# Kernel optimization log

Measured on AMD Instinct MI355X. Metric: run time of the kernel, lower is better.

## Reference

```python
import jax, jax.numpy as jnp
import numpy as np

N, E = 25000, 400000
D_NODE, D_EDGE_IN, D_EH, D_H, D_DUAL = 128, 16, 128, 256, 128


def layer_norm(x, g, b, eps=1e-5):
    mu = jnp.mean(x, axis=-1, keepdims=True)
    var = jnp.mean((x - mu) ** 2, axis=-1, keepdims=True)
    return (x - mu) * jax.lax.rsqrt(var + eps) * g + b


def setup_inputs() -> dict:
    key = jax.random.key(0)
    ks = jax.random.split(key, 20)

    def w(k, shape):
        return (jax.random.normal(k, shape, dtype=jnp.float32) * 0.05)

    inp = {
        "node_embedding": jax.random.normal(ks[0], (N, D_NODE), dtype=jnp.float32),
        "edge_index": jax.random.randint(ks[1], (2, E), 0, N, dtype=jnp.int64),
        "edge_attr": jax.random.normal(ks[2], (E, D_EDGE_IN), dtype=jnp.float32),
        "dual_node_emb": jax.random.normal(ks[3], (E, D_DUAL), dtype=jnp.float32),
        "atom_reactivity_logits": jax.random.normal(ks[4], (N,), dtype=jnp.float32),
        "W_be1": w(ks[5], (D_EDGE_IN, D_EH)), "b_be1": jnp.zeros((D_EH,), jnp.float32),
        "g_be1": jnp.ones((D_EH,), jnp.float32), "bb_be1": jnp.zeros((D_EH,), jnp.float32),
        "W_be2": w(ks[6], (D_EH, D_EH)), "b_be2": jnp.zeros((D_EH,), jnp.float32),
        "g_be2": jnp.ones((D_EH,), jnp.float32), "bb_be2": jnp.zeros((D_EH,), jnp.float32),
        "W_be3": w(ks[7], (D_EH, D_EH)), "b_be3": jnp.zeros((D_EH,), jnp.float32),
        "g_be3": jnp.ones((D_EH,), jnp.float32), "bb_be3": jnp.zeros((D_EH,), jnp.float32),
        # DualGraphBondReactivityPredictor
        "W_d1": w(ks[8], (D_DUAL, D_H)), "b_d1": jnp.zeros((D_H,), jnp.float32),
        "W_d2": w(ks[9], (D_H, D_H)), "b_d2": jnp.zeros((D_H,), jnp.float32),
        "W_do": w(ks[10], (D_H, 1)), "b_do": jnp.zeros((1,), jnp.float32),
        # main head: in = 2*D_NODE + D_EH + 3 = 387
        "W_f1": w(ks[11], (2 * D_NODE + D_EH + 3, D_H)), "b_f1": jnp.zeros((D_H,), jnp.float32),
        "W_f2": w(ks[12], (D_H, D_H)), "b_f2": jnp.zeros((D_H,), jnp.float32),
        "W_bo": w(ks[13], (D_H, 1)), "b_bo": jnp.zeros((1,), jnp.float32),
    }
    return inp


def reference(node_embedding, edge_index, edge_attr, dual_node_emb, atom_reactivity_logits,
              W_be1, b_be1, g_be1, bb_be1, W_be2, b_be2, g_be2, bb_be2,
              W_be3, b_be3, g_be3, bb_be3,
              W_d1, b_d1, W_d2, b_d2, W_do, b_do,
              W_f1, b_f1, W_f2, b_f2, W_bo, b_bo):
    src, dst = edge_index[0], edge_index[1]

    # BondEmbedding (dropout = identity in eval mode)
    e = jax.nn.silu(layer_norm(edge_attr @ W_be1 + b_be1, g_be1, bb_be1))
    e = jax.nn.silu(layer_norm(e @ W_be2 + b_be2, g_be2, bb_be2))
    e = jax.nn.silu(layer_norm(e @ W_be3 + b_be3, g_be3, bb_be3))  # [E, D_EH]

    atom_p = jax.nn.sigmoid(atom_reactivity_logits)  # [N]
    p_src = atom_p[src][:, None]  # [E,1]
    p_dst = atom_p[dst][:, None]

    # dual-graph bond reactivity
    d = jax.nn.silu(dual_node_emb @ W_d1 + b_d1)
    d = jax.nn.silu(d @ W_d2 + b_d2)
    dual_p = jax.nn.sigmoid((d @ W_do + b_do)[:, 0])[:, None]  # [E,1]

    feats = jnp.concatenate(
        [node_embedding[src], node_embedding[dst], e, dual_p, p_src, p_dst], axis=-1
    )  # [E, 2*D_NODE + D_EH + 3]

    x = jax.nn.silu(feats @ W_f1 + b_f1)
    x = jax.nn.silu(x @ W_f2 + b_f2)
    return (x @ W_bo + b_bo)[:, 0]  # [E]
```

## Files before the change

### kernel.cpp

```cpp
#include <hip/hip_runtime.h>
#include <hip/hip_bf16.h>
#include <stdint.h>

typedef __attribute__((ext_vector_type(8))) short bf16x8;
typedef __attribute__((ext_vector_type(4))) float f32x4;
typedef __attribute__((ext_vector_type(4))) float float4v;

__device__ __forceinline__ uint16_t bfc(float x){
    __hip_bfloat16 h = __float2bfloat16(x);
    return __builtin_bit_cast(uint16_t, h);
}
__device__ __forceinline__ uint32_t pk2(float a, float b){
    return (uint32_t)bfc(a) | ((uint32_t)bfc(b) << 16);
}
__device__ __forceinline__ float fsigmoid(float x){ return 1.0f / (1.0f + __expf(-x)); }
__device__ __forceinline__ float fsilu(float x){ return x * fsigmoid(x); }

__device__ __forceinline__ bf16x8 pack8(float4v lo, float4v hi){
    bf16x8 r;
    r[0]=(short)bfc(lo[0]); r[1]=(short)bfc(lo[1]);
    r[2]=(short)bfc(lo[2]); r[3]=(short)bfc(lo[3]);
    r[4]=(short)bfc(hi[0]); r[5]=(short)bfc(hi[1]);
    r[6]=(short)bfc(hi[2]); r[7]=(short)bfc(hi[3]);
    return r;
}

#define SZ_BE1 4096
#define SZ_128 16384
#define SZ_D1  32768
#define SZ_D2  65536
#define SZ_F1  98304
#define OFF_BE1 0
#define OFF_BE2 (OFF_BE1 + SZ_BE1)
#define OFF_BE3 (OFF_BE2 + SZ_128)
#define OFF_D1  (OFF_BE3 + SZ_128)
#define OFF_D2  (OFF_D1 + SZ_D1)
#define OFF_F1  (OFF_D2 + SZ_D2)
#define OFF_F2  (OFF_F1 + SZ_F1)
#define WS_ELEMS (OFF_F2 + SZ_D2)

__device__ __forceinline__ int fragpos(int k, int c, int OUT){
    int kt = k >> 5, ct = c >> 4;
    int fid = kt * (OUT >> 4) + ct;
    int ln = ((k & 31) >> 3) * 16 + (c & 15);
    return fid * 512 + ln * 8 + (k & 7);
}

__global__ void __launch_bounds__(256)
prep_w(const float* __restrict__ Wbe1, const float* __restrict__ Wbe2,
       const float* __restrict__ Wbe3, const float* __restrict__ Wd1,
       const float* __restrict__ Wd2,  const float* __restrict__ Wf1,
       const float* __restrict__ Wf2,  uint16_t* __restrict__ ws){
    int t = blockIdx.x * 256 + threadIdx.x;
    if (t >= WS_ELEMS) return;
    if (t < OFF_BE2) {
        int u = t;            int k = u >> 7, c = u & 127;
        float v = (k < 16) ? Wbe1[k * 128 + c] : 0.0f;
        ws[OFF_BE1 + fragpos(k, c, 128)] = bfc(v);
    } else if (t < OFF_BE3) {
        int u = t - OFF_BE2;  int k = u >> 7, c = u & 127;
        ws[OFF_BE2 + fragpos(k, c, 128)] = bfc(Wbe2[u]);
    } else if (t < OFF_D1) {
        int u = t - OFF_BE3;  int k = u >> 7, c = u & 127;
        ws[OFF_BE3 + fragpos(k, c, 128)] = bfc(Wbe3[u]);
    } else if (t < OFF_D2) {
        int u = t - OFF_D1;   int k = u >> 8, c = u & 255;
        ws[OFF_D1 + fragpos(k, c, 256)] = bfc(Wd1[u]);
    } else if (t < OFF_F1) {
        int u = t - OFF_D2;   int k = u >> 8, c = u & 255;
        ws[OFF_D2 + fragpos(k, c, 256)] = bfc(Wd2[u]);
    } else if (t < OFF_F2) {
        int u = t - OFF_F1;   int k = u >> 8, c = u & 255;
        ws[OFF_F1 + fragpos(k, c, 256)] = bfc(Wf1[u]);
    } else {
        int u = t - OFF_F2;   int k = u >> 8, c = u & 255;
        ws[OFF_F2 + fragpos(k, c, 256)] = bfc(Wf2[u]);
    }
}

__global__ void __launch_bounds__(256)
prep_n(const float* __restrict__ src, uint16_t* __restrict__ dst, int n){
    int t = blockIdx.x * 256 + threadIdx.x;
    if (t < n) dst[t] = bfc(src[t]);
}

typedef const __attribute__((address_space(1))) void gas_void;
typedef __attribute__((address_space(3))) void las_void;
__device__ __forceinline__ void g2l16(const void* g, void* l){
    __builtin_amdgcn_global_load_lds((gas_void*)g, (las_void*)l, 16, 0, 0);
}

#define LDS_TOTAL 135168

__global__ void __launch_bounds__(1024) __attribute__((amdgpu_waves_per_eu(4, 4)))
bond_fast_kernel(const int* __restrict__ edge_index,
                 const float* __restrict__ edge_attr, const float* __restrict__ dual_emb,
                 const float* __restrict__ logits,
                 const float* __restrict__ b_be1, const float* __restrict__ g_be1, const float* __restrict__ bb_be1,
                 const float* __restrict__ b_be2, const float* __restrict__ g_be2, const float* __restrict__ bb_be2,
                 const float* __restrict__ b_be3, const float* __restrict__ g_be3, const float* __restrict__ bb_be3,
                 const float* __restrict__ b_d1, const float* __restrict__ b_d2,
                 const float* __restrict__ W_do, const float* __restrict__ b_do,
                 const float* __restrict__ W_f1, const float* __restrict__ b_f1,
                 const float* __restrict__ b_f2,
                 const float* __restrict__ W_bo, const float* __restrict__ b_bo,
                 const uint16_t* __restrict__ ws, float* __restrict__ out, int E)
{
    __shared__ char lds[LDS_TOTAL];
    const int t    = threadIdx.x;
    const int wave = t >> 6;
    const int lane = t & 63;
    const int li   = lane & 15, lg = lane >> 4;
    const int eg   = wave >> 1;
    const int ch   = wave & 1;
    const int e0b  = blockIdx.x * 128;

    char* bufE = lds;
    char* h256 = lds + 32768;
    uint16_t* wb0 = (uint16_t*)(lds + 98304);
    uint16_t* wb1 = (uint16_t*)(lds + 114688);
    float* ps  = (float*)(lds + 131072);
    float* pd  = (float*)(lds + 131584);
    int* sidx  = (int*)(lds + 132096);
    int* didx  = (int*)(lds + 132608);
    float* dpp = (float*)(lds + 133120);
    float* bop = (float*)(lds + 134144);

    const uint8_t*  wsb = (const uint8_t*)ws;
    const uint16_t* nbf = ws + WS_ELEMS;

    if (t < 128) {
        int e = e0b + t; if (e >= E) e = E - 1;
        int s_ = edge_index[e];
        int d_ = edge_index[E + e];
        sidx[t] = s_; didx[t] = d_;
        ps[t] = fsigmoid(logits[s_]);
        pd[t] = fsigmoid(logits[d_]);
    }

    int cur = 0;
    auto stageW16 = [&](int elemoff){
        uint8_t* dst = (uint8_t*)(cur ? wb0 : wb1) + t * 16;
        g2l16(wsb + (size_t)elemoff * 2 + t * 16, dst);
    };
    auto stageW8 = [&](int elemoff){
        if (t >= 512){
            int u = t - 512;
            uint8_t* dst = (uint8_t*)(cur ? wb0 : wb1) + u * 16;
            g2l16(wsb + (size_t)elemoff * 2 + u * 16, dst);
        }
    };
    auto stepend = [&](){ __syncthreads(); cur ^= 1; };
    auto curbuf  = [&]() -> const uint16_t* { return cur ? wb1 : wb0; };

    f32x4 acc[8];

    auto ldf = [&](const uint16_t* w, int fid) -> bf16x8 {
        return *(const bf16x8*)(w + fid * 512 + lane * 8);
    };
    auto grpBE = [&](const uint16_t* w, bf16x8 a0){
        #pragma unroll
        for (int ct = 0; ct < 8; ++ct){
            bf16x8 b = ldf(w, ct);
            acc[ct] = __builtin_amdgcn_mfma_f32_16x16x32_bf16(a0, b, acc[ct], 0, 0, 0);
        }
    };
    auto grp256 = [&](const uint16_t* w, bf16x8 a0){
        #pragma unroll
        for (int ct = 0; ct < 8; ++ct){
            bf16x8 b = ldf(w, ch * 8 + ct);
            acc[ct] = __builtin_amdgcn_mfma_f32_16x16x32_bf16(a0, b, acc[ct], 0, 0, 0);
        }
    };
    auto initBE = [&](const float* b){
        #pragma unroll
        for (int ct = 0; ct < 8; ++ct){
            float bv = b[li + 16 * ct];
            f32x4 iv = {bv, bv, bv, bv};
            acc[ct] = iv;
        }
    };
    auto init256 = [&](const float* b){
        #pragma unroll
        for (int ct = 0; ct < 8; ++ct){
            float bv = b[ch * 128 + ct * 16 + li];
            f32x4 iv = {bv, bv, bv, bv};
            acc[ct] = iv;
        }
    };
    auto eb_read = [&](int row, int kt) -> bf16x8 {
        int off = row * 256 + (kt * 32 + lg * 8) * 2;
        return *(const bf16x8*)(bufE + (off ^ ((row & 7) << 4)));
    };
    auto h2_read = [&](int row, int kt) -> bf16x8 {
        int off = row * 512 + (kt * 32 + lg * 8) * 2;
        return *(const bf16x8*)(h256 + (off ^ ((row & 7) << 4)));
    };
    auto lnstoreBE = [&](const float* g, const float* bb){
        #pragma unroll
        for (int r = 0; r < 4; ++r){
            float s = 0.f, q = 0.f;
            #pragma unroll
            for (int ct = 0; ct < 8; ++ct){ float v = acc[ct][r]; s += v; q += v*v; }
            s += __shfl_xor(s, 1); q += __shfl_xor(q, 1);
            s += __shfl_xor(s, 2); q += __shfl_xor(q, 2);
            s += __shfl_xor(s, 4); q += __shfl_xor(q, 4);
            s += __shfl_xor(s, 8); q += __shfl_xor(q, 8);
            float mu = s * 0.0078125f;
            float var = q * 0.0078125f - mu * mu;
            float rs = rsqrtf(var + 1e-5f);
            int row = wave * 16 + lg * 4 + r;
            int rswz = (row & 7) << 4;
            #pragma unroll
            for (int ct = 0; ct < 8; ++ct){
                int col = li + 16 * ct;
                float v = (acc[ct][r] - mu) * rs * g[col] + bb[col];
                int off = row * 256 + col * 2;
                *(uint16_t*)(bufE + (off ^ rswz)) = bfc(fsilu(v));
            }
        }
    };
    auto silustore256 = [&](){
        #pragma unroll
        for (int r = 0; r < 4; ++r){
            int row = eg * 16 + lg * 4 + r;
            int rswz = (row & 7) << 4;
            #pragma unroll
            for (int ct = 0; ct < 8; ++ct){
                int off = row * 512 + (ch * 128 + ct * 16 + li) * 2;
                *(uint16_t*)(h256 + (off ^ rswz)) = bfc(fsilu(acc[ct][r]));
            }
        }
    };

    if (t >= 512){
        int u = t - 512;
        g2l16(wsb + u * 16, (uint8_t*)wb0 + u * 16);
    }
    __syncthreads();

    {
        stageW8(OFF_BE2);
        if (wave < 8){
            bf16x8 aE = {0,0,0,0,0,0,0,0};
            if (lg < 2){
                int ea = e0b + wave * 16 + li; if (ea >= E) ea = E - 1;
                const float* pa = edge_attr + (size_t)ea * 16 + lg * 8;
                aE = pack8(*(const float4v*)pa, *(const float4v*)(pa + 4));
            }
            initBE(b_be1);
            grpBE(curbuf(), aE);
            lnstoreBE(g_be1, bb_be1);
        }
        stepend();
    }

    if (wave < 8) initBE(b_be2);
    #pragma unroll 1
    for (int kt = 0; kt < 4; ++kt){
        if (kt < 3) stageW8(OFF_BE2 + (kt + 1) * 4096);
        else        stageW8(OFF_BE3);
        if (wave < 8){
            grpBE(curbuf(), eb_read(wave * 16 + li, kt));
            if (kt == 3) lnstoreBE(g_be2, bb_be2);
        }
        stepend();
    }
    if (wave < 8) initBE(b_be3);
    #pragma unroll 1
    for (int kt = 0; kt < 4; ++kt){
        if (kt < 3) stageW8(OFF_BE3 + (kt + 1) * 4096);
        else        stageW16(OFF_D1);
        if (wave < 8){
            grpBE(curbuf(), eb_read(wave * 16 + li, kt));
            if (kt == 3) lnstoreBE(g_be3, bb_be3);
        }
        stepend();
    }

    init256(b_d1);
    #pragma unroll 1
    for (int kt = 0; kt < 4; ++kt){
        float4v va0, va1;
        {
            int ea = e0b + eg * 16 + li; if (ea >= E) ea = E - 1;
            const float* pa = dual_emb + (size_t)ea * 128 + kt * 32 + lg * 8;
            va0 = *(const float4v*)pa; va1 = *(const float4v*)(pa + 4);
        }
        if (kt < 3) stageW16(OFF_D1 + (kt + 1) * 8192);
        else        stageW16(OFF_D2);
        grp256(curbuf(), pack8(va0, va1));
        if (kt == 3) silustore256();
        stepend();
    }

    init256(b_d2);
    #pragma unroll 1
    for (int kt = 0; kt < 8; ++kt){
        if (kt < 7) stageW16(OFF_D2 + (kt + 1) * 8192);
        else        stageW16(OFF_F1);
        grp256(curbuf(), h2_read(eg * 16 + li, kt));
        if (kt == 7){
            #pragma unroll
            for (int r = 0; r < 4; ++r){
                float s = 0.f;
                #pragma unroll
                for (int ct = 0; ct < 8; ++ct)
                    s += fsilu(acc[ct][r]) * W_do[ch * 128 + ct * 16 + li];
                s += __shfl_xor(s, 1); s += __shfl_xor(s, 2);
                s += __shfl_xor(s, 4); s += __shfl_xor(s, 8);
                if (li == 0) dpp[ch * 128 + eg * 16 + lg * 4 + r] = s;
            }
        }
        stepend();
    }

    {
        {
            float bdo0 = b_do[0];
            float dvv[4], psr[4], pdr[4];
            #pragma unroll
            for (int r = 0; r < 4; ++r){
                int row = eg * 16 + lg * 4 + r;
                dvv[r] = fsigmoid(dpp[row] + dpp[128 + row] + bdo0);
                psr[r] = ps[row]; pdr[r] = pd[row];
            }
            #pragma unroll
            for (int ct = 0; ct < 8; ++ct){
                int col = ch * 128 + ct * 16 + li;
                float bv = b_f1[col];
                float t0 = W_f1[384 * 256 + col];
                float t1 = W_f1[385 * 256 + col];
                float t2 = W_f1[386 * 256 + col];
                #pragma unroll
                for (int r = 0; r < 4; ++r)
                    acc[ct][r] = bv + dvv[r]*t0 + psr[r]*t1 + pdr[r]*t2;
            }
        }
        int s0 = sidx[eg * 16 + li];
        int d0 = didx[eg * 16 + li];
        #pragma unroll 1
        for (int kt = 0; kt < 12; ++kt){
            bf16x8 a0;
            if (kt < 8){
                int ra = (kt < 4) ? s0 : d0;
                int ko = (kt & 3) * 32 + lg * 8;
                a0 = *(const bf16x8*)(nbf + (size_t)ra * 128 + ko);
            } else {
                a0 = eb_read(eg * 16 + li, kt - 8);
            }
            if (kt < 11) stageW16(OFF_F1 + (kt + 1) * 8192);
            else         stageW16(OFF_F2);
            grp256(curbuf(), a0);
            if (kt == 11) silustore256();
            stepend();
        }
    }

    init256(b_f2);
    #pragma unroll 1
    for (int kt = 0; kt < 8; ++kt){
        if (kt < 7) stageW16(OFF_F2 + (kt + 1) * 8192);
        grp256(curbuf(), h2_read(eg * 16 + li, kt));
        if (kt == 7){
            #pragma unroll
            for (int r = 0; r < 4; ++r){
                float s = 0.f;
                #pragma unroll
                for (int ct = 0; ct < 8; ++ct)
                    s += fsilu(acc[ct][r]) * W_bo[ch * 128 + ct * 16 + li];
                s += __shfl_xor(s, 1); s += __shfl_xor(s, 2);
                s += __shfl_xor(s, 4); s += __shfl_xor(s, 8);
                if (li == 0) bop[ch * 128 + eg * 16 + lg * 4 + r] = s;
            }
        } else {
            stepend();
        }
    }
    __syncthreads();
    if (t < 128){
        int e = e0b + t;
        if (e < E) out[e] = bop[t] + bop[128 + t] + b_bo[0];
    }
}

#define LDS_TOTAL_FB 135168
__global__ void __launch_bounds__(512) __attribute__((amdgpu_waves_per_eu(2, 2)))
bond_fused_kernel(const float* __restrict__ node_emb, const int* __restrict__ edge_index,
                  const float* __restrict__ edge_attr, const float* __restrict__ dual_emb,
                  const float* __restrict__ logits,
                  const float* __restrict__ W_be1, const float* __restrict__ b_be1,
                  const float* __restrict__ g_be1, const float* __restrict__ bb_be1,
                  const float* __restrict__ W_be2, const float* __restrict__ b_be2,
                  const float* __restrict__ g_be2, const float* __restrict__ bb_be2,
                  const float* __restrict__ W_be3, const float* __restrict__ b_be3,
                  const float* __restrict__ g_be3, const float* __restrict__ bb_be3,
                  const float* __restrict__ W_d1, const float* __restrict__ b_d1,
                  const float* __restrict__ W_d2, const float* __restrict__ b_d2,
                  const float* __restrict__ W_do, const float* __restrict__ b_do,
                  const float* __restrict__ W_f1, const float* __restrict__ b_f1,
                  const float* __restrict__ W_f2, const float* __restrict__ b_f2,
                  const float* __restrict__ W_bo, const float* __restrict__ b_bo,
                  float* __restrict__ out, int E)
{
    __shared__ char lds[LDS_TOTAL_FB];
    const int t    = threadIdx.x;
    const int wave = t >> 6;
    const int lane = t & 63;
    const int li   = lane & 15, lg = lane >> 4;
    const int eg   = wave >> 1;
    const int ch   = wave & 1;
    const int e0b  = blockIdx.x * 128;

    char* bufE = lds;
    char* h256 = lds + 32768;
    uint16_t* wb0 = (uint16_t*)(lds + 98304);
    uint16_t* wb1 = (uint16_t*)(lds + 114688);
    float* ps  = (float*)(lds + 131072);
    float* pd  = (float*)(lds + 131584);
    int* sidx  = (int*)(lds + 132096);
    int* didx  = (int*)(lds + 132608);
    float* dpp = (float*)(lds + 133120);
    float* bop = (float*)(lds + 134144);

    if (t < 128) {
        int e = e0b + t; if (e >= E) e = E - 1;
        int s_ = edge_index[e];
        int d_ = edge_index[E + e];
        sidx[t] = s_; didx[t] = d_;
        ps[t] = fsigmoid(logits[s_]);
        pd[t] = fsigmoid(logits[d_]);
    }

    float sr[2][8];
    auto issueW256 = [&](const float* W, int kbase){
        #pragma unroll
        for (int h = 0; h < 2; ++h){
            const float* p = W + (size_t)(kbase + lg * 8) * 256 + (wave + 8*h) * 16 + li;
            #pragma unroll
            for (int j = 0; j < 8; ++j) sr[h][j] = p[j * 256];
        }
    };
    auto issueW128 = [&](const float* W, int kbase, int K){
        const float* p = W + (size_t)(kbase + lg * 8) * 128 + wave * 16 + li;
        #pragma unroll
        for (int j = 0; j < 8; ++j)
            sr[0][j] = (kbase + lg * 8 + j < K) ? p[j * 128] : 0.f;
    };
    auto commitW = [&](uint16_t* dst, int nh){
        #pragma unroll
        for (int h = 0; h < 2; ++h){
            if (h < nh){
                uint4 w;
                w.x = pk2(sr[h][0], sr[h][1]); w.y = pk2(sr[h][2], sr[h][3]);
                w.z = pk2(sr[h][4], sr[h][5]); w.w = pk2(sr[h][6], sr[h][7]);
                *(uint4*)(dst + (wave + 8*h) * 512 + lane * 8) = w;
            }
        }
    };

    int cur = 0;
    auto stepend = [&](int mode){
        if (mode) commitW(cur ? wb0 : wb1, mode == 128 ? 1 : 2);
        __syncthreads();
        cur ^= 1;
    };
    auto curbuf = [&]() -> const uint16_t* { return cur ? wb1 : wb0; };

    f32x4 acc[2][8];

    auto ldf = [&](const uint16_t* w, int fid) -> bf16x8 {
        return *(const bf16x8*)(w + fid * 512 + lane * 8);
    };
    auto grpBE = [&](const uint16_t* w, bf16x8 a0){
        #pragma unroll
        for (int ct = 0; ct < 8; ++ct){
            bf16x8 b = ldf(w, ct);
            acc[0][ct] = __builtin_amdgcn_mfma_f32_16x16x32_bf16(a0, b, acc[0][ct], 0, 0, 0);
        }
    };
    auto grp256 = [&](const uint16_t* w, bf16x8 a0, bf16x8 a1){
        #pragma unroll
        for (int ct = 0; ct < 8; ++ct){
            bf16x8 b = ldf(w, ch * 8 + ct);
            acc[0][ct] = __builtin_amdgcn_mfma_f32_16x16x32_bf16(a0, b, acc[0][ct], 0, 0, 0);
            acc[1][ct] = __builtin_amdgcn_mfma_f32_16x16x32_bf16(a1, b, acc[1][ct], 0, 0, 0);
        }
    };
    auto initBE = [&](const float* b){
        #pragma unroll
        for (int ct = 0; ct < 8; ++ct){
            float bv = b[li + 16 * ct];
            f32x4 iv = {bv, bv, bv, bv};
            acc[0][ct] = iv;
        }
    };
    auto init256 = [&](const float* b){
        #pragma unroll
        for (int ct = 0; ct < 8; ++ct){
            float bv = b[ch * 128 + ct * 16 + li];
            f32x4 iv = {bv, bv, bv, bv};
            acc[0][ct] = iv; acc[1][ct] = iv;
        }
    };
    auto eb_read = [&](int row, int kt) -> bf16x8 {
        int off = row * 256 + (kt * 32 + lg * 8) * 2;
        return *(const bf16x8*)(bufE + (off ^ ((row & 7) << 4)));
    };
    auto h2_read = [&](int row, int kt) -> bf16x8 {
        int off = row * 512 + (kt * 32 + lg * 8) * 2;
        return *(const bf16x8*)(h256 + (off ^ ((row & 7) << 4)));
    };
    auto lnstoreBE = [&](const float* g, const float* bb){
        #pragma unroll
        for (int r = 0; r < 4; ++r){
            float s = 0.f, q = 0.f;
            #pragma unroll
            for (int ct = 0; ct < 8; ++ct){ float v = acc[0][ct][r]; s += v; q += v*v; }
            s += __shfl_xor(s, 1); q += __shfl_xor(q, 1);
            s += __shfl_xor(s, 2); q += __shfl_xor(q, 2);
            s += __shfl_xor(s, 4); q += __shfl_xor(q, 4);
            s += __shfl_xor(s, 8); q += __shfl_xor(q, 8);
            float mu = s * 0.0078125f;
            float var = q * 0.0078125f - mu * mu;
            float rs = rsqrtf(var + 1e-5f);
            int row = wave * 16 + lg * 4 + r;
            int rswz = (row & 7) << 4;
            #pragma unroll
            for (int ct = 0; ct < 8; ++ct){
                int col = li + 16 * ct;
                float v = (acc[0][ct][r] - mu) * rs * g[col] + bb[col];
                int off = row * 256 + col * 2;
                *(uint16_t*)(bufE + (off ^ rswz)) = bfc(fsilu(v));
            }
        }
    };
    auto silustore256 = [&](){
        #pragma unroll
        for (int rt = 0; rt < 2; ++rt){
// ... 50 lines not shown
    init256(b_d1);
    #pragma unroll 1
    for (int kt = 0; kt < 4; ++kt){
        float4v va0, va1, vb0, vb1;
        {
            int ea = e0b + eg * 32 + li;      if (ea >= E) ea = E - 1;
            int eb = e0b + eg * 32 + 16 + li; if (eb >= E) eb = E - 1;
            const float* pa = dual_emb + (size_t)ea * 128 + kt * 32 + lg * 8;
            const float* pb = dual_emb + (size_t)eb * 128 + kt * 32 + lg * 8;
            va0 = *(const float4v*)pa; va1 = *(const float4v*)(pa + 4);
            vb0 = *(const float4v*)pb; vb1 = *(const float4v*)(pb + 4);
        }
        if (kt < 3) issueW256(W_d1, (kt + 1) * 32);
        else        issueW256(W_d2, 0);
        grp256(curbuf(), pack8(va0, va1), pack8(vb0, vb1));
        if (kt == 3) silustore256();
        stepend(256);
    }

    init256(b_d2);
    #pragma unroll 1
    for (int kt = 0; kt < 8; ++kt){
        if (kt < 7) issueW256(W_d2, (kt + 1) * 32);
        else        issueW256(W_f1, 0);
        grp256(curbuf(), h2_read(eg * 32 + li, kt), h2_read(eg * 32 + 16 + li, kt));
        if (kt == 7){
            #pragma unroll
            for (int rt = 0; rt < 2; ++rt){
                #pragma unroll
                for (int r = 0; r < 4; ++r){
                    float s = 0.f;
                    #pragma unroll
                    for (int ct = 0; ct < 8; ++ct)
                        s += fsilu(acc[rt][ct][r]) * W_do[ch * 128 + ct * 16 + li];
                    s += __shfl_xor(s, 1); s += __shfl_xor(s, 2);
                    s += __shfl_xor(s, 4); s += __shfl_xor(s, 8);
                    if (li == 0) dpp[ch * 128 + eg * 32 + rt * 16 + lg * 4 + r] = s;
                }
            }
        }
        stepend(256);
    }

    {
        {
            float bdo0 = b_do[0];
            #pragma unroll
            for (int ct = 0; ct < 8; ++ct){
                int col = ch * 128 + ct * 16 + li;
                float bv = b_f1[col];
                float t0 = W_f1[384 * 256 + col];
                float t1 = W_f1[385 * 256 + col];
                float t2 = W_f1[386 * 256 + col];
                #pragma unroll
                for (int rt = 0; rt < 2; ++rt)
                    #pragma unroll
                    for (int r = 0; r < 4; ++r){
                        int row = eg * 32 + rt * 16 + lg * 4 + r;
                        float dv = fsigmoid(dpp[row] + dpp[128 + row] + bdo0);
                        acc[rt][ct][r] = bv + dv*t0 + ps[row]*t1 + pd[row]*t2;
                    }
            }
        }
        int s0 = sidx[eg * 32 + li],      s1 = sidx[eg * 32 + 16 + li];
        int d0 = didx[eg * 32 + li],      d1 = didx[eg * 32 + 16 + li];
        #pragma unroll 1
        for (int kt = 0; kt < 12; ++kt){
            bf16x8 a0, a1;
            if (kt < 8){
                int ra = (kt < 4) ? s0 : d0;
                int rb = (kt < 4) ? s1 : d1;
                int ko = (kt & 3) * 32 + lg * 8;
                const float* pa = node_emb + (size_t)ra * 128 + ko;
                const float* pb = node_emb + (size_t)rb * 128 + ko;
                a0 = pack8(*(const float4v*)pa, *(const float4v*)(pa + 4));
                a1 = pack8(*(const float4v*)pb, *(const float4v*)(pb + 4));
            } else {
                a0 = eb_read(eg * 32 + li, kt - 8);
                a1 = eb_read(eg * 32 + 16 + li, kt - 8);
            }
            if (kt < 11) issueW256(W_f1, (kt + 1) * 32);
            else         issueW256(W_f2, 0);
            grp256(curbuf(), a0, a1);
            if (kt == 11) silustore256();
            stepend(256);
        }
    }

    init256(b_f2);
    #pragma unroll 1
    for (int kt = 0; kt < 8; ++kt){
        if (kt < 7) issueW256(W_f2, (kt + 1) * 32);
        grp256(curbuf(), h2_read(eg * 32 + li, kt), h2_read(eg * 32 + 16 + li, kt));
        if (kt == 7){
            #pragma unroll
            for (int rt = 0; rt < 2; ++rt){
                #pragma unroll
                for (int r = 0; r < 4; ++r){
                    float s = 0.f;
                    #pragma unroll
                    for (int ct = 0; ct < 8; ++ct)
                        s += fsilu(acc[rt][ct][r]) * W_bo[ch * 128 + ct * 16 + li];
                    s += __shfl_xor(s, 1); s += __shfl_xor(s, 2);
                    s += __shfl_xor(s, 4); s += __shfl_xor(s, 8);
                    if (li == 0) bop[ch * 128 + eg * 32 + rt * 16 + lg * 4 + r] = s;
                }
            }
        } else {
            stepend(256);
        }
    }
    __syncthreads();
    if (t < 128){
        int e = e0b + t;
        if (e < E) out[e] = bop[t] + bop[128 + t] + b_bo[0];
    }
}

extern "C" void kernel_launch(void* const* d_in, const int* in_sizes, int n_in,
                              void* d_out, int out_size, void* d_ws, size_t ws_size,
                              hipStream_t stream) {
    const float* node_emb   = (const float*)d_in[0];
    const int*   edge_index = (const int*)d_in[1];
    const float* edge_attr  = (const float*)d_in[2];
    const float* dual_emb   = (const float*)d_in[3];
    const float* logits     = (const float*)d_in[4];
    const float* W_be1 = (const float*)d_in[5];
    const float* b_be1 = (const float*)d_in[6];
    const float* g_be1 = (const float*)d_in[7];
    const float* bb_be1= (const float*)d_in[8];
    const float* W_be2 = (const float*)d_in[9];
    const float* b_be2 = (const float*)d_in[10];
    const float* g_be2 = (const float*)d_in[11];
    const float* bb_be2= (const float*)d_in[12];
    const float* W_be3 = (const float*)d_in[13];
    const float* b_be3 = (const float*)d_in[14];
    const float* g_be3 = (const float*)d_in[15];
    const float* bb_be3= (const float*)d_in[16];
    const float* W_d1  = (const float*)d_in[17];
    const float* b_d1  = (const float*)d_in[18];
    const float* W_d2  = (const float*)d_in[19];
    const float* b_d2  = (const float*)d_in[20];
    const float* W_do  = (const float*)d_in[21];
    const float* b_do  = (const float*)d_in[22];
    const float* W_f1  = (const float*)d_in[23];
    const float* b_f1  = (const float*)d_in[24];
    const float* W_f2  = (const float*)d_in[25];
    const float* b_f2  = (const float*)d_in[26];
    const float* W_bo  = (const float*)d_in[27];
    const float* b_bo  = (const float*)d_in[28];
    float* out = (float*)d_out;

    int E = in_sizes[2] / 16;
    int nblocks = (E + 127) / 128;
    size_t nodeElems = (size_t)in_sizes[0];
    size_t wsNeed = ((size_t)WS_ELEMS + nodeElems) * 2;

    if (ws_size >= wsNeed) {
        uint16_t* ws16 = (uint16_t*)d_ws;
        prep_w<<<dim3((WS_ELEMS + 255) / 256), dim3(256), 0, stream>>>(
            W_be1, W_be2, W_be3, W_d1, W_d2, W_f1, W_f2, ws16);
        prep_n<<<dim3((int)((nodeElems + 255) / 256)), dim3(256), 0, stream>>>(
            node_emb, ws16 + WS_ELEMS, (int)nodeElems);
        bond_fast_kernel<<<dim3(nblocks), dim3(1024), 0, stream>>>(
            edge_index, edge_attr, dual_emb, logits,
            b_be1, g_be1, bb_be1,
            b_be2, g_be2, bb_be2,
            b_be3, g_be3, bb_be3,
            b_d1, b_d2, W_do, b_do,
            W_f1, b_f1, b_f2, W_bo, b_bo,
            ws16, out, E);
    } else {
        bond_fused_kernel<<<dim3(nblocks), dim3(512), 0, stream>>>(
            node_emb, edge_index, edge_attr, dual_emb, logits,
            W_be1, b_be1, g_be1, bb_be1,
            W_be2, b_be2, g_be2, bb_be2,
            W_be3, b_be3, g_be3, bb_be3,
            W_d1, b_d1, W_d2, b_d2, W_do, b_do,
            W_f1, b_f1, W_f2, b_f2, W_bo, b_bo,
            out, E);
    }
}
```

Baseline: 805.5 us.

## Retile 256-wide GEMMs so each wave computes 32 rows by 64 columns

In the fast bond kernel, each wave now covers 32 edges and 64 output columns instead of 16 edges and 128 columns for the 256-wide layers (dual MLP and main head). Each weight fragment read from LDS is reused across two row tiles, so LDS weight traffic per MFMA is halved. In exchange, each wave loads twice as many A-operands, including the gathered node embeddings. The partial reductions for dual_p and the output grow to four column slices, which enlarges the LDS scratch.

```diff
diff --git a/kernel.cpp b/kernel.cpp
--- a/kernel.cpp
+++ b/kernel.cpp
@@ -90,7 +90,7 @@
     __builtin_amdgcn_global_load_lds((gas_void*)g, (las_void*)l, 16, 0, 0);
 }
 
-#define LDS_TOTAL 135168
+#define LDS_TOTAL 137216
 
 __global__ void __launch_bounds__(1024) __attribute__((amdgpu_waves_per_eu(4, 4)))
 bond_fast_kernel(const int* __restrict__ edge_index,
@@ -111,8 +111,8 @@
     const int wave = t >> 6;
     const int lane = t & 63;
     const int li   = lane & 15, lg = lane >> 4;
-    const int eg   = wave >> 1;
-    const int ch   = wave & 1;
+    const int eg   = wave >> 2;
+    const int ch   = wave & 3;
     const int e0b  = blockIdx.x * 128;
 
     char* bufE = lds;
@@ -124,7 +124,7 @@
     int* sidx  = (int*)(lds + 132096);
     int* didx  = (int*)(lds + 132608);
     float* dpp = (float*)(lds + 133120);
-    float* bop = (float*)(lds + 134144);
+    float* bop = (float*)(lds + 135168);
 
     const uint8_t*  wsb = (const uint8_t*)ws;
     const uint16_t* nbf = ws + WS_ELEMS;
@@ -165,11 +165,12 @@
             acc[ct] = __builtin_amdgcn_mfma_f32_16x16x32_bf16(a0, b, acc[ct], 0, 0, 0);
         }
     };
-    auto grp256 = [&](const uint16_t* w, bf16x8 a0){
-        #pragma unroll
-        for (int ct = 0; ct < 8; ++ct){
-            bf16x8 b = ldf(w, ch * 8 + ct);
-            acc[ct] = __builtin_amdgcn_mfma_f32_16x16x32_bf16(a0, b, acc[ct], 0, 0, 0);
+    auto grp256 = [&](const uint16_t* w, bf16x8 a0, bf16x8 a1){
+        #pragma unroll
+        for (int ct = 0; ct < 4; ++ct){
+            bf16x8 b = ldf(w, ch * 4 + ct);
+            acc[ct]     = __builtin_amdgcn_mfma_f32_16x16x32_bf16(a0, b, acc[ct],     0, 0, 0);
+            acc[4 + ct] = __builtin_amdgcn_mfma_f32_16x16x32_bf16(a1, b, acc[4 + ct], 0, 0, 0);
         }
     };
     auto initBE = [&](const float* b){
@@ -182,10 +183,10 @@
     };
     auto init256 = [&](const float* b){
         #pragma unroll
-        for (int ct = 0; ct < 8; ++ct){
-            float bv = b[ch * 128 + ct * 16 + li];
+        for (int ct = 0; ct < 4; ++ct){
+            float bv = b[ch * 64 + ct * 16 + li];
             f32x4 iv = {bv, bv, bv, bv};
-            acc[ct] = iv;
+            acc[ct] = iv; acc[4 + ct] = iv;
         }
     };
     auto eb_read = [&](int row, int kt) -> bf16x8 {
@@ -222,13 +223,16 @@
     };
     auto silustore256 = [&](){
         #pragma unroll
-        for (int r = 0; r < 4; ++r){
-            int row = eg * 16 + lg * 4 + r;
-            int rswz = (row & 7) << 4;
-            #pragma unroll
-            for (int ct = 0; ct < 8; ++ct){
-                int off = row * 512 + (ch * 128 + ct * 16 + li) * 2;
-                *(uint16_t*)(h256 + (off ^ rswz)) = bfc(fsilu(acc[ct][r]));
+        for (int rt = 0; rt < 2; ++rt){
+            #pragma unroll
+            for (int r = 0; r < 4; ++r){
+                int row = eg * 32 + rt * 16 + lg * 4 + r;
+                int rswz = (row & 7) << 4;
+                #pragma unroll
+                for (int ct = 0; ct < 4; ++ct){
+                    int off = row * 512 + (ch * 64 + ct * 16 + li) * 2;
+                    *(uint16_t*)(h256 + (off ^ rswz)) = bfc(fsilu(acc[rt * 4 + ct][r]));
+                }
             }
         }
     };
@@ -281,15 +285,18 @@
     init256(b_d1);
     #pragma unroll 1
     for (int kt = 0; kt < 4; ++kt){
-        float4v va0, va1;
-        {
-            int ea = e0b + eg * 16 + li; if (ea >= E) ea = E - 1;
-            const float* pa = dual_emb + (size_t)ea * 128 + kt * 32 + lg * 8;
-            va0 = *(const float4v*)pa; va1 = *(const float4v*)(pa + 4);
-        }
         if (kt < 3) stageW16(OFF_D1 + (kt + 1) * 8192);
         else        stageW16(OFF_D2);
-        grp256(curbuf(), pack8(va0, va1));
+        float4v va0, va1, vb0, vb1;
+        {
+            int ea = e0b + eg * 32 + li;      if (ea >= E) ea = E - 1;
+            int eb = e0b + eg * 32 + 16 + li; if (eb >= E) eb = E - 1;
+            const float* pa = dual_emb + (size_t)ea * 128 + kt * 32 + lg * 8;
+            const float* pb = dual_emb + (size_t)eb * 128 + kt * 32 + lg * 8;
+            va0 = *(const float4v*)pa; va1 = *(const float4v*)(pa + 4);
+            vb0 = *(const float4v*)pb; vb1 = *(const float4v*)(pb + 4);
+        }
+        grp256(curbuf(), pack8(va0, va1), pack8(vb0, vb1));
         if (kt == 3) silustore256();
         stepend();
     }
@@ -299,17 +306,20 @@
     for (int kt = 0; kt < 8; ++kt){
         if (kt < 7) stageW16(OFF_D2 + (kt + 1) * 8192);
         else        stageW16(OFF_F1);
-        grp256(curbuf(), h2_read(eg * 16 + li, kt));
+        grp256(curbuf(), h2_read(eg * 32 + li, kt), h2_read(eg * 32 + 16 + li, kt));
         if (kt == 7){
             #pragma unroll
-            for (int r = 0; r < 4; ++r){
-                float s = 0.f;
-                #pragma unroll
-                for (int ct = 0; ct < 8; ++ct)
-                    s += fsilu(acc[ct][r]) * W_do[ch * 128 + ct * 16 + li];
-                s += __shfl_xor(s, 1); s += __shfl_xor(s, 2);
-                s += __shfl_xor(s, 4); s += __shfl_xor(s, 8);
-                if (li == 0) dpp[ch * 128 + eg * 16 + lg * 4 + r] = s;
+            for (int rt = 0; rt < 2; ++rt){
+                #pragma unroll
+                for (int r = 0; r < 4; ++r){
+                    float s = 0.f;
+                    #pragma unroll
+                    for (int ct = 0; ct < 4; ++ct)
+                        s += fsilu(acc[rt * 4 + ct][r]) * W_do[ch * 64 + ct * 16 + li];
+                    s += __shfl_xor(s, 1); s += __shfl_xor(s, 2);
+                    s += __shfl_xor(s, 4); s += __shfl_xor(s, 8);
+                    if (li == 0) dpp[ch * 128 + eg * 32 + rt * 16 + lg * 4 + r] = s;
+                }
             }
         }
         stepend();
@@ -318,40 +328,48 @@
     {
         {
             float bdo0 = b_do[0];
-            float dvv[4], psr[4], pdr[4];
-            #pragma unroll
-            for (int r = 0; r < 4; ++r){
-                int row = eg * 16 + lg * 4 + r;
-                dvv[r] = fsigmoid(dpp[row] + dpp[128 + row] + bdo0);
-                psr[r] = ps[row]; pdr[r] = pd[row];
-            }
-            #pragma unroll
-            for (int ct = 0; ct < 8; ++ct){
-                int col = ch * 128 + ct * 16 + li;
+            float dvv[2][4];
+            #pragma unroll
+            for (int rt = 0; rt < 2; ++rt)
+                #pragma unroll
+                for (int r = 0; r < 4; ++r){
+                    int row = eg * 32 + rt * 16 + lg * 4 + r;
+                    dvv[rt][r] = fsigmoid(dpp[row] + dpp[128 + row] + dpp[256 + row] + dpp[384 + row] + bdo0);
+                }
+            #pragma unroll
+            for (int ct = 0; ct < 4; ++ct){
+                int col = ch * 64 + ct * 16 + li;
                 float bv = b_f1[col];
                 float t0 = W_f1[384 * 256 + col];
                 float t1 = W_f1[385 * 256 + col];
                 float t2 = W_f1[386 * 256 + col];
                 #pragma unroll
-                for (int r = 0; r < 4; ++r)
-                    acc[ct][r] = bv + dvv[r]*t0 + psr[r]*t1 + pdr[r]*t2;
-            }
-        }
-        int s0 = sidx[eg * 16 + li];
-        int d0 = didx[eg * 16 + li];
+                for (int rt = 0; rt < 2; ++rt)
+                    #pragma unroll
+                    for (int r = 0; r < 4; ++r){
+                        int row = eg * 32 + rt * 16 + lg * 4 + r;
+                        acc[rt * 4 + ct][r] = bv + dvv[rt][r]*t0 + ps[row]*t1 + pd[row]*t2;
+                    }
+            }
+        }
+        int s0 = sidx[eg * 32 + li],      s1 = sidx[eg * 32 + 16 + li];
+        int d0 = didx[eg * 32 + li],      d1 = didx[eg * 32 + 16 + li];
         #pragma unroll 1
         for (int kt = 0; kt < 12; ++kt){
-            bf16x8 a0;
+            if (kt < 11) stageW16(OFF_F1 + (kt + 1) * 8192);
+            else         stageW16(OFF_F2);
+            bf16x8 a0, a1;
             if (kt < 8){
                 int ra = (kt < 4) ? s0 : d0;
+                int rb = (kt < 4) ? s1 : d1;
                 int ko = (kt & 3) * 32 + lg * 8;
                 a0 = *(const bf16x8*)(nbf + (size_t)ra * 128 + ko);
+                a1 = *(const bf16x8*)(nbf + (size_t)rb * 128 + ko);
             } else {
-                a0 = eb_read(eg * 16 + li, kt - 8);
-            }
-            if (kt < 11) stageW16(OFF_F1 + (kt + 1) * 8192);
-            else         stageW16(OFF_F2);
-            grp256(curbuf(), a0);
+                a0 = eb_read(eg * 32 + li, kt - 8);
+                a1 = eb_read(eg * 32 + 16 + li, kt - 8);
+            }
+            grp256(curbuf(), a0, a1);
             if (kt == 11) silustore256();
             stepend();
         }
@@ -361,17 +379,20 @@
     #pragma unroll 1
     for (int kt = 0; kt < 8; ++kt){
         if (kt < 7) stageW16(OFF_F2 + (kt + 1) * 8192);
-        grp256(curbuf(), h2_read(eg * 16 + li, kt));
+        grp256(curbuf(), h2_read(eg * 32 + li, kt), h2_read(eg * 32 + 16 + li, kt));
         if (kt == 7){
             #pragma unroll
-            for (int r = 0; r < 4; ++r){
-                float s = 0.f;
-                #pragma unroll
-                for (int ct = 0; ct < 8; ++ct)
-                    s += fsilu(acc[ct][r]) * W_bo[ch * 128 + ct * 16 + li];
-                s += __shfl_xor(s, 1); s += __shfl_xor(s, 2);
-                s += __shfl_xor(s, 4); s += __shfl_xor(s, 8);
-                if (li == 0) bop[ch * 128 + eg * 16 + lg * 4 + r] = s;
+            for (int rt = 0; rt < 2; ++rt){
+                #pragma unroll
+                for (int r = 0; r < 4; ++r){
+                    float s = 0.f;
+                    #pragma unroll
+                    for (int ct = 0; ct < 4; ++ct)
+                        s += fsilu(acc[rt * 4 + ct][r]) * W_bo[ch * 64 + ct * 16 + li];
+                    s += __shfl_xor(s, 1); s += __shfl_xor(s, 2);
+                    s += __shfl_xor(s, 4); s += __shfl_xor(s, 8);
+                    if (li == 0) bop[ch * 128 + eg * 32 + rt * 16 + lg * 4 + r] = s;
+                }
             }
         } else {
             stepend();
@@ -380,7 +401,7 @@
     __syncthreads();
     if (t < 128){
         int e = e0b + t;
-        if (e < E) out[e] = bop[t] + bop[128 + t] + b_bo[0];
+        if (e < E) out[e] = bop[t] + bop[128 + t] + bop[256 + t] + bop[384 + t] + b_bo[0];
     }
 }
 
```

New measurement: 873.0 us. +8.4%, slower.

## Shrink fast kernel blocks to 64 edges and 512 threads with half-tile weight staging

Applied to the files above, without the earlier changes.

Blocks now handle 64 edges with 512 threads, and LDS use drops to about 66KB so more blocks fit per CU. Weight staging goes from 8KB steps to 4KB half-steps, and each k-step is split into two MFMA groups of four. The 256-wide weight fragment layout is permuted to match this split. The aim is higher occupancy and smaller LDS, at the cost of twice as many barriers and each staged weight tile being reused across fewer edges.

```diff
diff --git a/kernel.cpp b/kernel.cpp
--- a/kernel.cpp
+++ b/kernel.cpp
@@ -39,9 +39,15 @@
 #define OFF_F2  (OFF_F1 + SZ_F1)
 #define WS_ELEMS (OFF_F2 + SZ_D2)
 
-__device__ __forceinline__ int fragpos(int k, int c, int OUT){
-    int kt = k >> 5, ct = c >> 4;
-    int fid = kt * (OUT >> 4) + ct;
+__device__ __forceinline__ int fragpos128(int k, int c){
+    int fid = (k >> 5) * 8 + (c >> 4);
+    int ln = ((k & 31) >> 3) * 16 + (c & 15);
+    return fid * 512 + ln * 8 + (k & 7);
+}
+__device__ __forceinline__ int fragpos256(int k, int c){
+    int ct = c >> 4;
+    int pos = (ct & 3) + ((ct >> 2) & 1) * 8 + ((ct >> 3) & 1) * 4;
+    int fid = (k >> 5) * 16 + pos;
     int ln = ((k & 31) >> 3) * 16 + (c & 15);
     return fid * 512 + ln * 8 + (k & 7);
 }
@@ -56,25 +62,25 @@
     if (t < OFF_BE2) {
         int u = t;            int k = u >> 7, c = u & 127;
         float v = (k < 16) ? Wbe1[k * 128 + c] : 0.0f;
-        ws[OFF_BE1 + fragpos(k, c, 128)] = bfc(v);
+        ws[OFF_BE1 + fragpos128(k, c)] = bfc(v);
     } else if (t < OFF_BE3) {
         int u = t - OFF_BE2;  int k = u >> 7, c = u & 127;
-        ws[OFF_BE2 + fragpos(k, c, 128)] = bfc(Wbe2[u]);
+        ws[OFF_BE2 + fragpos128(k, c)] = bfc(Wbe2[u]);
     } else if (t < OFF_D1) {
         int u = t - OFF_BE3;  int k = u >> 7, c = u & 127;
-        ws[OFF_BE3 + fragpos(k, c, 128)] = bfc(Wbe3[u]);
+        ws[OFF_BE3 + fragpos128(k, c)] = bfc(Wbe3[u]);
     } else if (t < OFF_D2) {
         int u = t - OFF_D1;   int k = u >> 8, c = u & 255;
-        ws[OFF_D1 + fragpos(k, c, 256)] = bfc(Wd1[u]);
+        ws[OFF_D1 + fragpos256(k, c)] = bfc(Wd1[u]);
     } else if (t < OFF_F1) {
         int u = t - OFF_D2;   int k = u >> 8, c = u & 255;
-        ws[OFF_D2 + fragpos(k, c, 256)] = bfc(Wd2[u]);
+        ws[OFF_D2 + fragpos256(k, c)] = bfc(Wd2[u]);
     } else if (t < OFF_F2) {
         int u = t - OFF_F1;   int k = u >> 8, c = u & 255;
-        ws[OFF_F1 + fragpos(k, c, 256)] = bfc(Wf1[u]);
+        ws[OFF_F1 + fragpos256(k, c)] = bfc(Wf1[u]);
     } else {
         int u = t - OFF_F2;   int k = u >> 8, c = u & 255;
-        ws[OFF_F2 + fragpos(k, c, 256)] = bfc(Wf2[u]);
+        ws[OFF_F2 + fragpos256(k, c)] = bfc(Wf2[u]);
     }
 }
 
@@ -90,9 +96,9 @@
     __builtin_amdgcn_global_load_lds((gas_void*)g, (las_void*)l, 16, 0, 0);
 }
 
-#define LDS_TOTAL 135168
-
-__global__ void __launch_bounds__(1024) __attribute__((amdgpu_waves_per_eu(4, 4)))
+#define LDS_FAST 67840
+
+__global__ void __launch_bounds__(512, 4)
 bond_fast_kernel(const int* __restrict__ edge_index,
                  const float* __restrict__ edge_attr, const float* __restrict__ dual_emb,
                  const float* __restrict__ logits,
@@ -106,30 +112,31 @@
                  const float* __restrict__ W_bo, const float* __restrict__ b_bo,
                  const uint16_t* __restrict__ ws, float* __restrict__ out, int E)
 {
-    __shared__ char lds[LDS_TOTAL];
+    __shared__ char lds[LDS_FAST];
     const int t    = threadIdx.x;
     const int wave = t >> 6;
     const int lane = t & 63;
     const int li   = lane & 15, lg = lane >> 4;
     const int eg   = wave >> 1;
     const int ch   = wave & 1;
-    const int e0b  = blockIdx.x * 128;
+    const int e0b  = blockIdx.x * 64;
 
     char* bufE = lds;
-    char* h256 = lds + 32768;
-    uint16_t* wb0 = (uint16_t*)(lds + 98304);
-    uint16_t* wb1 = (uint16_t*)(lds + 114688);
-    float* ps  = (float*)(lds + 131072);
-    float* pd  = (float*)(lds + 131584);
-    int* sidx  = (int*)(lds + 132096);
-    int* didx  = (int*)(lds + 132608);
-    float* dpp = (float*)(lds + 133120);
-    float* bop = (float*)(lds + 134144);
+    char* h256 = lds + 16384;
+    uint16_t* wb0 = (uint16_t*)(lds + 49152);
+    uint16_t* wb1 = (uint16_t*)(lds + 57344);
+    float* ps  = (float*)(lds + 65536);
+    float* pd  = (float*)(lds + 65792);
+    int* sidx  = (int*)(lds + 66048);
+    int* didx  = (int*)(lds + 66304);
+    float* dpp = (float*)(lds + 66560);
+    float* bop = (float*)(lds + 67072);
+    float* dpv = (float*)(lds + 67584);
 
     const uint8_t*  wsb = (const uint8_t*)ws;
     const uint16_t* nbf = ws + WS_ELEMS;
 
-    if (t < 128) {
+    if (t < 64) {
         int e = e0b + t; if (e >= E) e = E - 1;
         int s_ = edge_index[e];
         int d_ = edge_index[E + e];
@@ -139,38 +146,25 @@
     }
 
     int cur = 0;
-    auto stageW16 = [&](int elemoff){
+    auto stageN = [&](int elemoff){
         uint8_t* dst = (uint8_t*)(cur ? wb0 : wb1) + t * 16;
         g2l16(wsb + (size_t)elemoff * 2 + t * 16, dst);
     };
-    auto stageW8 = [&](int elemoff){
-        if (t >= 512){
-            int u = t - 512;
-            uint8_t* dst = (uint8_t*)(cur ? wb0 : wb1) + u * 16;
-            g2l16(wsb + (size_t)elemoff * 2 + u * 16, dst);
-        }
-    };
     auto stepend = [&](){ __syncthreads(); cur ^= 1; };
-    auto curbuf  = [&]() -> const uint16_t* { return cur ? wb1 : wb0; };
+    auto curb    = [&]() -> const uint16_t* { return cur ? wb1 : wb0; };
 
     f32x4 acc[8];
 
     auto ldf = [&](const uint16_t* w, int fid) -> bf16x8 {
         return *(const bf16x8*)(w + fid * 512 + lane * 8);
     };
-    auto grpBE = [&](const uint16_t* w, bf16x8 a0){
-        #pragma unroll
-        for (int ct = 0; ct < 8; ++ct){
-            bf16x8 b = ldf(w, ct);
-            acc[ct] = __builtin_amdgcn_mfma_f32_16x16x32_bf16(a0, b, acc[ct], 0, 0, 0);
-        }
-    };
-    auto grp256 = [&](const uint16_t* w, bf16x8 a0){
-        #pragma unroll
-        for (int ct = 0; ct < 8; ++ct){
-            bf16x8 b = ldf(w, ch * 8 + ct);
-            acc[ct] = __builtin_amdgcn_mfma_f32_16x16x32_bf16(a0, b, acc[ct], 0, 0, 0);
-        }
+    auto eb_read = [&](int row, int kt) -> bf16x8 {
+        int off = row * 256 + (kt * 32 + lg * 8) * 2;
+        return *(const bf16x8*)(bufE + (off ^ ((row & 7) << 4)));
+    };
+    auto h2_read = [&](int row, int kt) -> bf16x8 {
+        int off = row * 512 + (kt * 32 + lg * 8) * 2;
+        return *(const bf16x8*)(h256 + (off ^ ((row & 7) << 4)));
     };
     auto initBE = [&](const float* b){
         #pragma unroll
@@ -182,19 +176,23 @@
     };
     auto init256 = [&](const float* b){
         #pragma unroll
-        for (int ct = 0; ct < 8; ++ct){
-            float bv = b[ch * 128 + ct * 16 + li];
+        for (int j = 0; j < 8; ++j){
+            float bv = b[ch * 128 + j * 16 + li];
             f32x4 iv = {bv, bv, bv, bv};
-            acc[ct] = iv;
-        }
-    };
-    auto eb_read = [&](int row, int kt) -> bf16x8 {
-        int off = row * 256 + (kt * 32 + lg * 8) * 2;
-        return *(const bf16x8*)(bufE + (off ^ ((row & 7) << 4)));
-    };
-    auto h2_read = [&](int row, int kt) -> bf16x8 {
-        int off = row * 512 + (kt * 32 + lg * 8) * 2;
-        return *(const bf16x8*)(h256 + (off ^ ((row & 7) << 4)));
+            acc[j] = iv;
+        }
+    };
+    auto mfma4lo = [&](bf16x8 a){
+        acc[0] = __builtin_amdgcn_mfma_f32_16x16x32_bf16(a, ldf(curb(), ch*4+0), acc[0], 0, 0, 0);
+        acc[1] = __builtin_amdgcn_mfma_f32_16x16x32_bf16(a, ldf(curb(), ch*4+1), acc[1], 0, 0, 0);
+        acc[2] = __builtin_amdgcn_mfma_f32_16x16x32_bf16(a, ldf(curb(), ch*4+2), acc[2], 0, 0, 0);
+        acc[3] = __builtin_amdgcn_mfma_f32_16x16x32_bf16(a, ldf(curb(), ch*4+3), acc[3], 0, 0, 0);
+    };
+    auto mfma4hi = [&](bf16x8 a){
+        acc[4] = __builtin_amdgcn_mfma_f32_16x16x32_bf16(a, ldf(curb(), ch*4+0), acc[4], 0, 0, 0);
+        acc[5] = __builtin_amdgcn_mfma_f32_16x16x32_bf16(a, ldf(curb(), ch*4+1), acc[5], 0, 0, 0);
+        acc[6] = __builtin_amdgcn_mfma_f32_16x16x32_bf16(a, ldf(curb(), ch*4+2), acc[6], 0, 0, 0);
+        acc[7] = __builtin_amdgcn_mfma_f32_16x16x32_bf16(a, ldf(curb(), ch*4+3), acc[7], 0, 0, 0);
     };
     auto lnstoreBE = [&](const float* g, const float* bb){
         #pragma unroll
@@ -226,53 +224,55 @@
             int row = eg * 16 + lg * 4 + r;
             int rswz = (row & 7) << 4;
             #pragma unroll
-            for (int ct = 0; ct < 8; ++ct){
-                int off = row * 512 + (ch * 128 + ct * 16 + li) * 2;
-                *(uint16_t*)(h256 + (off ^ rswz)) = bfc(fsilu(acc[ct][r]));
-            }
-        }
-    };
-
-    if (t >= 512){
-        int u = t - 512;
-        g2l16(wsb + u * 16, (uint8_t*)wb0 + u * 16);
-    }
+            for (int j = 0; j < 8; ++j){
+                int off = row * 512 + (ch * 128 + j * 16 + li) * 2;
+                *(uint16_t*)(h256 + (off ^ rswz)) = bfc(fsilu(acc[j][r]));
+            }
+        }
+    };
+
+    g2l16(wsb + t * 16, (uint8_t*)wb0 + t * 16);
     __syncthreads();
 
     {
-        stageW8(OFF_BE2);
-        if (wave < 8){
+        stageN(OFF_BE2);
+        if (wave < 4){
+            initBE(b_be1);
             bf16x8 aE = {0,0,0,0,0,0,0,0};
             if (lg < 2){
                 int ea = e0b + wave * 16 + li; if (ea >= E) ea = E - 1;
                 const float* pa = edge_attr + (size_t)ea * 16 + lg * 8;
                 aE = pack8(*(const float4v*)pa, *(const float4v*)(pa + 4));
             }
-            initBE(b_be1);
-            grpBE(curbuf(), aE);
+            #pragma unroll
+            for (int ct = 0; ct < 8; ++ct)
+                acc[ct] = __builtin_amdgcn_mfma_f32_16x16x32_bf16(aE, ldf(curb(), ct), acc[ct], 0, 0, 0);
             lnstoreBE(g_be1, bb_be1);
         }
         stepend();
     }
-
-    if (wave < 8) initBE(b_be2);
+    if (wave < 4) initBE(b_be2);
     #pragma unroll 1
     for (int kt = 0; kt < 4; ++kt){
-        if (kt < 3) stageW8(OFF_BE2 + (kt + 1) * 4096);
-        else        stageW8(OFF_BE3);
-        if (wave < 8){
-            grpBE(curbuf(), eb_read(wave * 16 + li, kt));
+        stageN(kt < 3 ? OFF_BE2 + (kt + 1) * 4096 : OFF_BE3);
+        if (wave < 4){
+            bf16x8 a = eb_read(wave * 16 + li, kt);
+            #pragma unroll
+            for (int ct = 0; ct < 8; ++ct)
+                acc[ct] = __builtin_amdgcn_mfma_f32_16x16x32_bf16(a, ldf(curb(), ct), acc[ct], 0, 0, 0);
             if (kt == 3) lnstoreBE(g_be2, bb_be2);
         }
         stepend();
     }
-    if (wave < 8) initBE(b_be3);
+    if (wave < 4) initBE(b_be3);
     #pragma unroll 1
     for (int kt = 0; kt < 4; ++kt){
-        if (kt < 3) stageW8(OFF_BE3 + (kt + 1) * 4096);
-        else        stageW16(OFF_D1);
-        if (wave < 8){
-            grpBE(curbuf(), eb_read(wave * 16 + li, kt));
+        stageN(kt < 3 ? OFF_BE3 + (kt + 1) * 4096 : OFF_D1);
+        if (wave < 4){
+            bf16x8 a = eb_read(wave * 16 + li, kt);
+            #pragma unroll
+            for (int ct = 0; ct < 8; ++ct)
+                acc[ct] = __builtin_amdgcn_mfma_f32_16x16x32_bf16(a, ldf(curb(), ct), acc[ct], 0, 0, 0);
             if (kt == 3) lnstoreBE(g_be3, bb_be3);
         }
         stepend();
@@ -281,15 +281,17 @@
     init256(b_d1);
     #pragma unroll 1
     for (int kt = 0; kt < 4; ++kt){
-        float4v va0, va1;
+        stageN(OFF_D1 + (2 * kt + 1) * 4096);
+        bf16x8 aD;
         {
             int ea = e0b + eg * 16 + li; if (ea >= E) ea = E - 1;
             const float* pa = dual_emb + (size_t)ea * 128 + kt * 32 + lg * 8;
-            va0 = *(const float4v*)pa; va1 = *(const float4v*)(pa + 4);
-        }
-        if (kt < 3) stageW16(OFF_D1 + (kt + 1) * 8192);
-        else        stageW16(OFF_D2);
-        grp256(curbuf(), pack8(va0, va1));
+            aD = pack8(*(const float4v*)pa, *(const float4v*)(pa + 4));
+        }
+        mfma4lo(aD);
+        stepend();
+        stageN(kt < 3 ? OFF_D1 + (2 * kt + 2) * 4096 : OFF_D2);
+        mfma4hi(aD);
         if (kt == 3) silustore256();
         stepend();
     }
@@ -297,61 +299,62 @@
     init256(b_d2);
     #pragma unroll 1
     for (int kt = 0; kt < 8; ++kt){
-        if (kt < 7) stageW16(OFF_D2 + (kt + 1) * 8192);
-        else        stageW16(OFF_F1);
-        grp256(curbuf(), h2_read(eg * 16 + li, kt));
+        stageN(OFF_D2 + (2 * kt + 1) * 4096);
+        bf16x8 aD = h2_read(eg * 16 + li, kt);
+        mfma4lo(aD);
+        stepend();
+        stageN(kt < 7 ? OFF_D2 + (2 * kt + 2) * 4096 : OFF_F1);
+        mfma4hi(aD);
         if (kt == 7){
             #pragma unroll
             for (int r = 0; r < 4; ++r){
                 float s = 0.f;
                 #pragma unroll
-                for (int ct = 0; ct < 8; ++ct)
-                    s += fsilu(acc[ct][r]) * W_do[ch * 128 + ct * 16 + li];
+                for (int j = 0; j < 8; ++j)
+                    s += fsilu(acc[j][r]) * W_do[ch * 128 + j * 16 + li];
                 s += __shfl_xor(s, 1); s += __shfl_xor(s, 2);
                 s += __shfl_xor(s, 4); s += __shfl_xor(s, 8);
-                if (li == 0) dpp[ch * 128 + eg * 16 + lg * 4 + r] = s;
-            }
-        }
-        stepend();
-    }
+                if (li == 0) dpp[ch * 64 + eg * 16 + lg * 4 + r] = s;
+            }
+        }
+        stepend();
+    }
+    if (t < 64) dpv[t] = fsigmoid(dpp[t] + dpp[64 + t] + b_do[0]);
+    __syncthreads();
 
     {
+        int sv = sidx[eg * 16 + li];
+        int dv = didx[eg * 16 + li];
         {
-            float bdo0 = b_do[0];
             float dvv[4], psr[4], pdr[4];
             #pragma unroll
             for (int r = 0; r < 4; ++r){
                 int row = eg * 16 + lg * 4 + r;
-                dvv[r] = fsigmoid(dpp[row] + dpp[128 + row] + bdo0);
-                psr[r] = ps[row]; pdr[r] = pd[row];
-            }
-            #pragma unroll
-            for (int ct = 0; ct < 8; ++ct){
-                int col = ch * 128 + ct * 16 + li;
+                dvv[r] = dpv[row]; psr[r] = ps[row]; pdr[r] = pd[row];
+            }
+            #pragma unroll
+            for (int j = 0; j < 8; ++j){
+                int col = ch * 128 + j * 16 + li;
                 float bv = b_f1[col];
                 float t0 = W_f1[384 * 256 + col];
                 float t1 = W_f1[385 * 256 + col];
                 float t2 = W_f1[386 * 256 + col];
                 #pragma unroll
                 for (int r = 0; r < 4; ++r)
-                    acc[ct][r] = bv + dvv[r]*t0 + psr[r]*t1 + pdr[r]*t2;
-            }
-        }
-        int s0 = sidx[eg * 16 + li];
-        int d0 = didx[eg * 16 + li];
+                    acc[j][r] = bv + dvv[r]*t0 + psr[r]*t1 + pdr[r]*t2;
+            }
+        }
         #pragma unroll 1
         for (int kt = 0; kt < 12; ++kt){
-            bf16x8 a0;
-            if (kt < 8){
-                int ra = (kt < 4) ? s0 : d0;
-                int ko = (kt & 3) * 32 + lg * 8;
-                a0 = *(const bf16x8*)(nbf + (size_t)ra * 128 + ko);
-            } else {
-                a0 = eb_read(eg * 16 + li, kt - 8);
-            }
-            if (kt < 11) stageW16(OFF_F1 + (kt + 1) * 8192);
-            else         stageW16(OFF_F2);
-            grp256(curbuf(), a0);
+            stageN(OFF_F1 + (2 * kt + 1) * 4096);
+            bf16x8 aD;
+            if (kt < 4)      aD = *(const bf16x8*)(nbf + (size_t)sv * 128 + kt * 32 + lg * 8);
+            else if (kt < 8) aD = *(const bf16x8*)(nbf + (size_t)dv * 128 + (kt - 4) * 32 + lg * 8);
+            else             aD = eb_read(eg * 16 + li, kt - 8);
+            mfma4lo(aD);
+            stepend();
+            stageN(kt < 11 ? OFF_F1 + (2 * kt + 2) * 4096 : OFF_F2);
+            mfma4hi(aD);
             if (kt == 11) silustore256();
             stepend();
         }
@@ -360,31 +363,39 @@
     init256(b_f2);
     #pragma unroll 1
     for (int kt = 0; kt < 8; ++kt){
-        if (kt < 7) stageW16(OFF_F2 + (kt + 1) * 8192);
-        grp256(curbuf(), h2_read(eg * 16 + li, kt));
+        stageN(OFF_F2 + (2 * kt + 1) * 4096);
+        bf16x8 aD = h2_read(eg * 16 + li, kt);
+        mfma4lo(aD);
+        stepend();
+        if (kt < 7) stageN(OFF_F2 + (2 * kt + 2) * 4096);
+        mfma4hi(aD);
         if (kt == 7){
             #pragma unroll
             for (int r = 0; r < 4; ++r){
                 float s = 0.f;
                 #pragma unroll
-                for (int ct = 0; ct < 8; ++ct)
-                    s += fsilu(acc[ct][r]) * W_bo[ch * 128 + ct * 16 + li];
+                for (int j = 0; j < 8; ++j)
+                    s += fsilu(acc[j][r]) * W_bo[ch * 128 + j * 16 + li];
                 s += __shfl_xor(s, 1); s += __shfl_xor(s, 2);
                 s += __shfl_xor(s, 4); s += __shfl_xor(s, 8);
-                if (li == 0) bop[ch * 128 + eg * 16 + lg * 4 + r] = s;
-            }
-        } else {
-            stepend();
-        }
-    }
-    __syncthreads();
-    if (t < 128){
+                if (li == 0) bop[ch * 64 + eg * 16 + lg * 4 + r] = s;
+            }
+        }
+        stepend();
+    }
+    if (t < 64){
         int e = e0b + t;
-        if (e < E) out[e] = bop[t] + bop[128 + t] + b_bo[0];
+        if (e < E) out[e] = bop[t] + bop[64 + t] + b_bo[0];
     }
 }
 
 #define LDS_TOTAL_FB 135168
+__device__ __forceinline__ int fragpos_fb(int k, int c, int OUT){
+    int kt = k >> 5, ct = c >> 4;
+    int fid = kt * (OUT >> 4) + ct;
+    int ln = ((k & 31) >> 3) * 16 + (c & 15);
+    return fid * 512 + ln * 8 + (k & 7);
+}
 __global__ void __launch_bounds__(512) __attribute__((amdgpu_waves_per_eu(2, 2)))
 bond_fused_kernel(const float* __restrict__ node_emb, const int* __restrict__ edge_index,
                   const float* __restrict__ edge_attr, const float* __restrict__ dual_emb,
@@ -741,7 +752,6 @@
     float* out = (float*)d_out;
 
     int E = in_sizes[2] / 16;
-    int nblocks = (E + 127) / 128;
     size_t nodeElems = (size_t)in_sizes[0];
     size_t wsNeed = ((size_t)WS_ELEMS + nodeElems) * 2;
 
@@ -751,7 +761,8 @@
             W_be1, W_be2, W_be3, W_d1, W_d2, W_f1, W_f2, ws16);
         prep_n<<<dim3((int)((nodeElems + 255) / 256)), dim3(256), 0, stream>>>(
             node_emb, ws16 + WS_ELEMS, (int)nodeElems);
-        bond_fast_kernel<<<dim3(nblocks), dim3(1024), 0, stream>>>(
+        int nblocks = (E + 63) / 64;
+        bond_fast_kernel<<<dim3(nblocks), dim3(512), 0, stream>>>(
             edge_index, edge_attr, dual_emb, logits,
             b_be1, g_be1, bb_be1,
             b_be2, g_be2, bb_be2,
@@ -760,6 +771,7 @@
             W_f1, b_f1, b_f2, W_bo, b_bo,
             ws16, out, E);
     } else {
+        int nblocks = (E + 127) / 128;
         bond_fused_kernel<<<dim3(nblocks), dim3(512), 0, stream>>>(
             node_emb, edge_index, edge_attr, dual_emb, logits,
             W_be1, b_be1, g_be1, bb_be1,
```

Result: no change. 803.3 us (-0.3%).
